# Kernel optimization log

Measured on AMD Instinct MI355X. Metric: run time of the kernel, lower is better.

## Reference

```python
import jax, jax.numpy as jnp
import numpy as np

WS = 7          # window_size
DIM = 384
H = 12          # num_heads
N = WS * WS     # tokens per window
NW = 64         # number of windows (attn_mask.shape[0])
B_ = 4096       # window-batch; divisible by NW


def _relative_position_index(ws: int) -> np.ndarray:
    coords = np.stack(np.meshgrid(np.arange(ws), np.arange(ws), indexing='ij'))  # (2, ws, ws)
    flat = coords.reshape(2, -1)                                                 # (2, N)
    rel = flat[:, :, None] - flat[:, None, :]                                    # (2, N, N)
    rel = rel.transpose(1, 2, 0).astype(np.int64)                                # (N, N, 2)
    rel[:, :, 0] += ws - 1
    rel[:, :, 1] += ws - 1
    rel[:, :, 0] *= 2 * ws - 1
    return rel.sum(-1)                                                           # (N, N)

REL_IDX = jnp.asarray(_relative_position_index(WS))


def setup_inputs() -> dict:
    key = jax.random.key(0)
    ks = jax.random.split(key, 7)
    return {
        'x': jax.random.normal(ks[0], (B_, N, DIM), jnp.float32),
        'attn_mask': jax.random.normal(ks[1], (NW, N, N), jnp.float32),
        'qkv_w': jax.random.normal(ks[2], (3 * DIM, DIM), jnp.float32) * 0.02,
        'qkv_b': jax.random.normal(ks[3], (3 * DIM,), jnp.float32) * 0.02,
        'proj_w': jax.random.normal(ks[4], (DIM, DIM), jnp.float32) * 0.02,
        'proj_b': jax.random.normal(ks[5], (DIM,), jnp.float32) * 0.02,
        'rpb_table': jax.random.normal(ks[6], ((2 * WS - 1) ** 2, H), jnp.float32) * 0.02,
    }


def reference(x, attn_mask, qkv_w, qkv_b, proj_w, proj_b, rpb_table):
    b, n, c = x.shape
    hd = c // H
    scale = hd ** (-0.5)
    qkv = x @ qkv_w.T + qkv_b                                  # (B_, N, 3C)
    qkv = qkv.reshape(b, n, 3, H, hd).transpose(2, 0, 3, 1, 4)  # (3, B_, H, N, hd)
    q, k, v = qkv[0] * scale, qkv[1], qkv[2]
    attn = jnp.einsum('bhnd,bhmd->bhnm', q, k)                 # (B_, H, N, N)
    bias = rpb_table[REL_IDX]                                  # (N, N, H)
    attn = attn + bias.transpose(2, 0, 1)[None]
    nw = attn_mask.shape[0]
    attn = attn.reshape(b // nw, nw, H, n, n) + attn_mask[None, :, None]
    attn = jax.nn.softmax(attn.reshape(b, H, n, n), axis=-1)
    out = jnp.einsum('bhnm,bhmd->bhnd', attn, v)               # (B_, H, N, hd)
    out = out.transpose(0, 2, 1, 3).reshape(b, n, c)
    return out @ proj_w.T + proj_b
```

## Files before the change

### kernel.cpp

```cpp
#include <hip/hip_runtime.h>

#define TOKS 49
#define DIM_ 384
#define NHEAD 12

typedef short bf16x8 __attribute__((ext_vector_type(8)));
typedef float f32x4 __attribute__((ext_vector_type(4)));

#define SXA 392
#define SQK 136
#define SV   72

#define LDS_ELEMS (64*SXA + 64*SQK + 64*SQK + 128*SV + 64*SXA)
#define LDS_BYTES (LDS_ELEMS*2)

#define W1E (3*DIM_*DIM_)
#define W2E (DIM_*DIM_)
#define CMBE (64*NHEAD*64*64)
#define WS_NEEDED ((size_t)(W1E+W2E)*2 + (size_t)CMBE*4)

__device__ __forceinline__ unsigned short f2b(float f) {
  union { float f; unsigned u; } x; x.f = f;
  return (unsigned short)((x.u + 0x7FFFu + ((x.u >> 16) & 1u)) >> 16);
}

__device__ __forceinline__ unsigned pack2(float lo, float hi) {
  return (unsigned)f2b(lo) | ((unsigned)f2b(hi) << 16);
}

__global__ void prep_kernel(const float* __restrict__ qkv_w,
                            const float* __restrict__ proj_w,
                            const float* __restrict__ rpb,
                            const float* __restrict__ mask,
                            unsigned short* __restrict__ w1p,
                            unsigned short* __restrict__ w2p,
                            float* __restrict__ cmb) {
  int i = blockIdx.x * 256 + threadIdx.x;
  if (i < W1E) {
    int j = i & 7, l = (i >> 3) & 63, rest = i >> 9;
    int kk = rest % 12, ct = rest / 12;
    w1p[i] = f2b(qkv_w[(ct*16 + (l & 15))*DIM_ + kk*32 + ((l >> 4) << 3) + j]);
  }
  if (i < W2E) {
    int j = i & 7, l = (i >> 3) & 63, rest = i >> 9;
    int kk = rest % 12, ct = rest / 12;
    w2p[i] = f2b(proj_w[(ct*16 + (l & 15))*DIM_ + kk*32 + ((l >> 4) << 3) + j]);
  }
  if (i < CMBE) {
    int k = i & 63, q = (i >> 6) & 63, hw = i >> 12;
    int h = hw % 12, wi = hw / 12;
    float v = -1e30f;
    if (q < TOKS && k < TOKS) {
      int idx = (q/7 - k/7 + 6)*13 + (q%7 - k%7 + 6);
      v = rpb[idx*NHEAD + h] + mask[((size_t)wi*TOKS + q)*TOKS + k];
    }
    cmb[i] = v;
  }
}

__global__ __launch_bounds__(1024, 1)
void wattn_kernel(const float* __restrict__ x,
                  const unsigned short* __restrict__ w1p,
                  const float* __restrict__ b1,
                  const unsigned short* __restrict__ w2p,
                  const float* __restrict__ b2,
                  const float* __restrict__ cmb,
                  float* __restrict__ out) {
  extern __shared__ unsigned short lds[];
  unsigned short* xA  = lds;
  unsigned short* Q4  = xA + 64*SXA;
  unsigned short* K4  = Q4 + 64*SQK;
  unsigned short* Vt4 = K4 + 64*SQK;
  unsigned short* Ob  = Vt4 + 128*SV;

  const int tid  = threadIdx.x;
  const int lane = tid & 63;
  const int wv   = tid >> 6;
  const int lr   = lane & 15;
  const int lg   = lane >> 4;
  const int b    = blockIdx.x;
  const int wi   = b & 63;

  const int mh    = wv & 1;
  const int ctile = wv >> 1;

  {
    const float* xg = x + (size_t)b * TOKS * DIM_;
    for (int idx = tid; idx < TOKS*48; idx += 1024) {
      int r = idx / 48, c8 = (idx % 48) << 3;
      const float4* p = (const float4*)(xg + r*DIM_ + c8);
      float4 a0 = p[0], a1 = p[1];
      uint4 w;
      w.x = pack2(a0.x, a0.y); w.y = pack2(a0.z, a0.w);
      w.z = pack2(a1.x, a1.y); w.w = pack2(a1.z, a1.w);
      *(uint4*)&xA[r*SXA + c8] = w;
    }
    uint4 z = {0,0,0,0};
    for (int idx = tid; idx < 15*48; idx += 1024) {
      int r = 49 + idx / 48, c8 = (idx % 48) << 3;
      *(uint4*)&xA[r*SXA + c8] = z;
    }
  }
  __syncthreads();

  const f32x4 fz = {0.f, 0.f, 0.f, 0.f};
  f32x4 aq[2], ak[2], av[2];

  auto g1c = [&](int gg) {
    const int cb = gg*8 + ctile;
    const unsigned short* bq = w1p + (size_t)(cb*12)*512 + (lane << 3);
    const unsigned short* bk = bq + (size_t)(24*12)*512;
    const unsigned short* bv = bq + (size_t)(48*12)*512;
    #pragma unroll
    for (int t = 0; t < 2; ++t) { aq[t] = fz; ak[t] = fz; av[t] = fz; }
    #pragma unroll
    for (int kk = 0; kk < 12; ++kk) {
      bf16x8 fq = *(const bf16x8*)(bq + kk*512);
      bf16x8 fk = *(const bf16x8*)(bk + kk*512);
      bf16x8 fv = *(const bf16x8*)(bv + kk*512);
      #pragma unroll
      for (int t = 0; t < 2; ++t) {
        bf16x8 a = *(const bf16x8*)&xA[((mh*2 + t)*16 + lr)*SXA + kk*32 + lg*8];
        aq[t] = __builtin_amdgcn_mfma_f32_16x16x32_bf16(fq, a, aq[t], 0, 0, 0);
        ak[t] = __builtin_amdgcn_mfma_f32_16x16x32_bf16(fk, a, ak[t], 0, 0, 0);
        av[t] = __builtin_amdgcn_mfma_f32_16x16x32_bf16(a, fv, av[t], 0, 0, 0);
      }
    }
  };

  auto g1w = [&](int gg) {
    const int cb = gg*8 + ctile;
    const f32x4 qb4 = *(const f32x4*)(b1 + cb*16 + (lg << 2));
    const f32x4 kb4 = *(const f32x4*)(b1 + (24 + cb)*16 + (lg << 2));
    const float bsv = b1[(48 + cb)*16 + lr];
    const int d128 = (ctile << 4) + lr;
    #pragma unroll
    for (int t = 0; t < 2; ++t) {
      const int tokr = mh*32 + t*16 + lr;
      uint2 qw, kw, vw;
      qw.x = pack2((aq[t][0] + qb4[0]) * 0.17677669529663687f,
                   (aq[t][1] + qb4[1]) * 0.17677669529663687f);
      qw.y = pack2((aq[t][2] + qb4[2]) * 0.17677669529663687f,
                   (aq[t][3] + qb4[3]) * 0.17677669529663687f);
      kw.x = pack2(ak[t][0] + kb4[0], ak[t][1] + kb4[1]);
      kw.y = pack2(ak[t][2] + kb4[2], ak[t][3] + kb4[3]);
      vw.x = pack2(av[t][0] + bsv, av[t][1] + bsv);
      vw.y = pack2(av[t][2] + bsv, av[t][3] + bsv);
      *(uint2*)&Q4[tokr*SQK + (ctile << 4) + (lg << 2)] = qw;
      *(uint2*)&K4[tokr*SQK + (ctile << 4) + (lg << 2)] = kw;
      *(uint2*)&Vt4[d128*SV + mh*32 + t*16 + (lg << 2)] = vw;
    }
  };

  for (int g = 0; g < 3; ++g) {
    g1c(g);
    g1w(g);
    __syncthreads();

    const int hl = wv >> 2;
    const int h  = g*4 + hl;
    const int qoff = hl * 32;
    const int m0 = (wv & 3) << 4;

    f32x4 c4[4];
    const float* cp = cmb + (((size_t)(wi*NHEAD + h)) << 12) + ((m0 + lr) << 6);
    #pragma unroll
    for (int nt = 0; nt < 4; ++nt)
      c4[nt] = *(const f32x4*)(cp + nt*16 + (lg << 2));

    bf16x8 qa = *(const bf16x8*)&Q4[(m0 + lr)*SQK + qoff + lg*8];
    f32x4 S[4];
    #pragma unroll
    for (int nt = 0; nt < 4; ++nt) {
      bf16x8 kb = *(const bf16x8*)&K4[((nt << 4) + lr)*SQK + qoff + lg*8];
      S[nt] = __builtin_amdgcn_mfma_f32_16x16x32_bf16(kb, qa, fz, 0, 0, 0);
    }

    float p[4][4];
    float mx = -1e30f;
    #pragma unroll
    for (int nt = 0; nt < 4; ++nt)
      #pragma unroll
      for (int jj = 0; jj < 4; ++jj) {
        p[nt][jj] = S[nt][jj] + c4[nt][jj];
        mx = fmaxf(mx, p[nt][jj]);
      }
    mx = fmaxf(mx, __shfl_xor(mx, 16));
    mx = fmaxf(mx, __shfl_xor(mx, 32));
    float sum = 0.f;
    #pragma unroll
    for (int nt = 0; nt < 4; ++nt)
      #pragma unroll
      for (int jj = 0; jj < 4; ++jj) {
        float e = __expf(p[nt][jj] - mx);
        p[nt][jj] = e; sum += e;
      }
    sum += __shfl_xor(sum, 16);
    sum += __shfl_xor(sum, 32);
    const float inv = 1.0f / sum;

    unsigned pk0[4], pk1[4];
    #pragma unroll
    for (int nt = 0; nt < 4; ++nt) {
      pk0[nt] = pack2(p[nt][0]*inv, p[nt][1]*inv);
      pk1[nt] = pack2(p[nt][2]*inv, p[nt][3]*inv);
    }

    const int src0 = lr + ((lane & 16) << 1);
    const int src1 = src0 + 16;
    const bool loH = lane < 32;
    f32x4 o0 = fz, o1 = fz;
    #pragma unroll
    for (int kk = 0; kk < 2; ++kk) {
      unsigned wA0 = __shfl(pk0[2*kk], src0), wB0 = __shfl(pk0[2*kk+1], src0);
      unsigned wA1 = __shfl(pk1[2*kk], src0), wB1 = __shfl(pk1[2*kk+1], src0);
      unsigned wA2 = __shfl(pk0[2*kk], src1), wB2 = __shfl(pk0[2*kk+1], src1);
      unsigned wA3 = __shfl(pk1[2*kk], src1), wB3 = __shfl(pk1[2*kk+1], src1);
      union { unsigned u[4]; bf16x8 v; } af;
      af.u[0] = loH ? wA0 : wB0;
      af.u[1] = loH ? wA1 : wB1;
      af.u[2] = loH ? wA2 : wB2;
      af.u[3] = loH ? wA3 : wB3;
      bf16x8 vb0 = *(const bf16x8*)&Vt4[(qoff + lr)*SV + kk*32 + lg*8];
      bf16x8 vb1 = *(const bf16x8*)&Vt4[(qoff + 16 + lr)*SV + kk*32 + lg*8];
      o0 = __builtin_amdgcn_mfma_f32_16x16x32_bf16(vb0, af.v, o0, 0, 0, 0);
      o1 = __builtin_amdgcn_mfma_f32_16x16x32_bf16(vb1, af.v, o1, 0, 0, 0);
    }
    const int orow = m0 + lr;
    uint2 w0, w1;
    w0.x = pack2(o0[0], o0[1]); w0.y = pack2(o0[2], o0[3]);
    w1.x = pack2(o1[0], o1[1]); w1.y = pack2(o1[2], o1[3]);
    *(uint2*)&Ob[orow*SXA + h*32 + (lg << 2)]      = w0;
    *(uint2*)&Ob[orow*SXA + h*32 + 16 + (lg << 2)] = w1;

    __syncthreads();
  }

  {
    const unsigned short* bp0 = w2p + (size_t)(ctile*12)*512 + (lane << 3);
    const unsigned short* bp1 = bp0 + (size_t)(8*12)*512;
    const unsigned short* bp2 = bp0 + (size_t)(16*12)*512;
    f32x4 ac0[2], ac1[2], ac2[2];
    #pragma unroll
    for (int t = 0; t < 2; ++t) { ac0[t] = fz; ac1[t] = fz; ac2[t] = fz; }
    #pragma unroll
    for (int kk = 0; kk < 12; ++kk) {
      bf16x8 f0 = *(const bf16x8*)(bp0 + kk*512);
      bf16x8 f1 = *(const bf16x8*)(bp1 + kk*512);
      bf16x8 f2 = *(const bf16x8*)(bp2 + kk*512);
      #pragma unroll
      for (int t = 0; t < 2; ++t) {
        bf16x8 ob = *(const bf16x8*)&Ob[((mh*2 + t)*16 + lr)*SXA + kk*32 + lg*8];
        ac0[t] = __builtin_amdgcn_mfma_f32_16x16x32_bf16(f0, ob, ac0[t], 0, 0, 0);
        ac1[t] = __builtin_amdgcn_mfma_f32_16x16x32_bf16(f1, ob, ac1[t], 0, 0, 0);
        ac2[t] = __builtin_amdgcn_mfma_f32_16x16x32_bf16(f2, ob, ac2[t], 0, 0, 0);
      }
    }
    float* og = out + (size_t)b * TOKS * DIM_;
    #pragma unroll
    for (int ni = 0; ni < 3; ++ni) {
      const int col0 = ((ctile + ni*8) << 4) + (lg << 2);
      const f32x4 pb = *(const f32x4*)(b2 + col0);
      const f32x4* ac = ni == 0 ? ac0 : (ni == 1 ? ac1 : ac2);
      #pragma unroll
      for (int t = 0; t < 2; ++t) {
        const int tok = (mh*2 + t)*16 + lr;
        if (tok < TOKS) {
          f32x4 v = ac[t] + pb;
          *(f32x4*)(og + tok*DIM_ + col0) = v;
        }
      }
    }
  }
}

extern "C" void kernel_launch(void* const* d_in, const int* in_sizes, int n_in,
                              void* d_out, int out_size, void* d_ws, size_t ws_size,
                              hipStream_t stream) {
  const float* x      = (const float*)d_in[0];
  const float* mask   = (const float*)d_in[1];
  const float* qkv_w  = (const float*)d_in[2];
  const float* qkv_b  = (const float*)d_in[3];
  const float* proj_w = (const float*)d_in[4];
  const float* proj_b = (const float*)d_in[5];
  const float* rpb    = (const float*)d_in[6];
  float* out = (float*)d_out;

  if (ws_size < WS_NEEDED) return;

  unsigned short* w1p = (unsigned short*)d_ws;
  unsigned short* w2p = w1p + W1E;
  float* cmb = (float*)(w2p + W2E);

  prep_kernel<<<(CMBE + 255)/256, 256, 0, stream>>>(qkv_w, proj_w, rpb, mask,
                                                    w1p, w2p, cmb);

  hipFuncSetAttribute((const void*)wattn_kernel,
                      hipFuncAttributeMaxDynamicSharedMemorySize, LDS_BYTES);
  wattn_kernel<<<4096, 1024, LDS_BYTES, stream>>>(x, w1p, qkv_b, w2p,
                                                  proj_b, cmb, out);
}
```

Measured before the change: 606.0 us.

## Shrink blocks to 512 threads and interleave per-head projection accumulation

Blocks drop from 1024 to 512 threads and process two heads per step across six steps instead of four heads across three. The output projection is no longer a final pass over a full attention-output buffer. It is accumulated step by step from a small per-step buffer that reuses the Q region, which shrinks LDS so several blocks can share a CU. The cost is more barriers per step, more accumulator registers per thread, and repeated small weight loads for the projection.

```diff
diff --git a/kernel.cpp b/kernel.cpp
--- a/kernel.cpp
+++ b/kernel.cpp
@@ -8,10 +8,9 @@
 typedef float f32x4 __attribute__((ext_vector_type(4)));
 
 #define SXA 392
-#define SQK 136
-#define SV   72
-
-#define LDS_ELEMS (64*SXA + 64*SQK + 64*SQK + 128*SV + 64*SXA)
+#define SQ  72
+
+#define LDS_ELEMS (64*SXA + 3*64*SQ)
 #define LDS_BYTES (LDS_ELEMS*2)
 
 #define W1E (3*DIM_*DIM_)
@@ -23,7 +22,6 @@
   union { float f; unsigned u; } x; x.f = f;
   return (unsigned short)((x.u + 0x7FFFu + ((x.u >> 16) & 1u)) >> 16);
 }
-
 __device__ __forceinline__ unsigned pack2(float lo, float hi) {
   return (unsigned)f2b(lo) | ((unsigned)f2b(hi) << 16);
 }
@@ -58,7 +56,7 @@
   }
 }
 
-__global__ __launch_bounds__(1024, 1)
+__global__ __launch_bounds__(512, 4)
 void wattn_kernel(const float* __restrict__ x,
                   const unsigned short* __restrict__ w1p,
                   const float* __restrict__ b1,
@@ -68,10 +66,10 @@
                   float* __restrict__ out) {
   extern __shared__ unsigned short lds[];
   unsigned short* xA  = lds;
-  unsigned short* Q4  = xA + 64*SXA;
-  unsigned short* K4  = Q4 + 64*SQK;
-  unsigned short* Vt4 = K4 + 64*SQK;
-  unsigned short* Ob  = Vt4 + 128*SV;
+  unsigned short* Q2  = xA + 64*SXA;
+  unsigned short* K2  = Q2 + 64*SQ;
+  unsigned short* Vt2 = K2 + 64*SQ;
+  unsigned short* ObG = Q2;
 
   const int tid  = threadIdx.x;
   const int lane = tid & 63;
@@ -81,12 +79,14 @@
   const int b    = blockIdx.x;
   const int wi   = b & 63;
 
-  const int mh    = wv & 1;
-  const int ctile = wv >> 1;
+  const int ct2 = wv >> 1;
+  const int mh  = wv & 1;
+  const int hl  = wv >> 2;
+  const int m0  = (wv & 3) << 4;
 
   {
     const float* xg = x + (size_t)b * TOKS * DIM_;
-    for (int idx = tid; idx < TOKS*48; idx += 1024) {
+    for (int idx = tid; idx < TOKS*48; idx += 512) {
       int r = idx / 48, c8 = (idx % 48) << 3;
       const float4* p = (const float4*)(xg + r*DIM_ + c8);
       float4 a0 = p[0], a1 = p[1];
@@ -96,7 +96,7 @@
       *(uint4*)&xA[r*SXA + c8] = w;
     }
     uint4 z = {0,0,0,0};
-    for (int idx = tid; idx < 15*48; idx += 1024) {
+    for (int idx = tid; idx < 15*48; idx += 512) {
       int r = 49 + idx / 48, c8 = (idx % 48) << 3;
       *(uint4*)&xA[r*SXA + c8] = z;
     }
@@ -104,63 +104,57 @@
   __syncthreads();
 
   const f32x4 fz = {0.f, 0.f, 0.f, 0.f};
-  f32x4 aq[2], ak[2], av[2];
-
-  auto g1c = [&](int gg) {
-    const int cb = gg*8 + ctile;
-    const unsigned short* bq = w1p + (size_t)(cb*12)*512 + (lane << 3);
-    const unsigned short* bk = bq + (size_t)(24*12)*512;
-    const unsigned short* bv = bq + (size_t)(48*12)*512;
-    #pragma unroll
-    for (int t = 0; t < 2; ++t) { aq[t] = fz; ak[t] = fz; av[t] = fz; }
-    #pragma unroll
-    for (int kk = 0; kk < 12; ++kk) {
-      bf16x8 fq = *(const bf16x8*)(bq + kk*512);
-      bf16x8 fk = *(const bf16x8*)(bk + kk*512);
-      bf16x8 fv = *(const bf16x8*)(bv + kk*512);
+  f32x4 ac0[4], ac1[4], ac2[4];
+  #pragma unroll
+  for (int m = 0; m < 4; ++m) { ac0[m]=fz; ac1[m]=fz; ac2[m]=fz; }
+
+  for (int g = 0; g < 6; ++g) {
+    {
+      const int cb = g*4 + ct2;
+      const unsigned short* bq = w1p + (size_t)(cb*12)*512 + (lane << 3);
+      const unsigned short* bk = bq + (size_t)(24*12)*512;
+      const unsigned short* bv = bq + (size_t)(48*12)*512;
+      f32x4 aq[2], ak[2], av[2];
+      #pragma unroll
+      for (int t = 0; t < 2; ++t) { aq[t]=fz; ak[t]=fz; av[t]=fz; }
+      #pragma unroll
+      for (int kk = 0; kk < 12; ++kk) {
+        bf16x8 fq = *(const bf16x8*)(bq + kk*512);
+        bf16x8 fk = *(const bf16x8*)(bk + kk*512);
+        bf16x8 fv = *(const bf16x8*)(bv + kk*512);
+        #pragma unroll
+        for (int t = 0; t < 2; ++t) {
+          bf16x8 a = *(const bf16x8*)&xA[((mh*2 + t)*16 + lr)*SXA + kk*32 + lg*8];
+          aq[t] = __builtin_amdgcn_mfma_f32_16x16x32_bf16(fq, a, aq[t], 0, 0, 0);
+          ak[t] = __builtin_amdgcn_mfma_f32_16x16x32_bf16(fk, a, ak[t], 0, 0, 0);
+          av[t] = __builtin_amdgcn_mfma_f32_16x16x32_bf16(a, fv, av[t], 0, 0, 0);
+        }
+      }
+      const f32x4 qb4 = *(const f32x4*)(b1 + cb*16 + (lg << 2));
+      const f32x4 kb4 = *(const f32x4*)(b1 + (24 + cb)*16 + (lg << 2));
+      const float bsv = b1[(48 + cb)*16 + lr];
+      const int d64 = (ct2 << 4) + lr;
       #pragma unroll
       for (int t = 0; t < 2; ++t) {
-        bf16x8 a = *(const bf16x8*)&xA[((mh*2 + t)*16 + lr)*SXA + kk*32 + lg*8];
-        aq[t] = __builtin_amdgcn_mfma_f32_16x16x32_bf16(fq, a, aq[t], 0, 0, 0);
-        ak[t] = __builtin_amdgcn_mfma_f32_16x16x32_bf16(fk, a, ak[t], 0, 0, 0);
-        av[t] = __builtin_amdgcn_mfma_f32_16x16x32_bf16(a, fv, av[t], 0, 0, 0);
-      }
-    }
-  };
-
-  auto g1w = [&](int gg) {
-    const int cb = gg*8 + ctile;
-    const f32x4 qb4 = *(const f32x4*)(b1 + cb*16 + (lg << 2));
-    const f32x4 kb4 = *(const f32x4*)(b1 + (24 + cb)*16 + (lg << 2));
-    const float bsv = b1[(48 + cb)*16 + lr];
-    const int d128 = (ctile << 4) + lr;
-    #pragma unroll
-    for (int t = 0; t < 2; ++t) {
-      const int tokr = mh*32 + t*16 + lr;
-      uint2 qw, kw, vw;
-      qw.x = pack2((aq[t][0] + qb4[0]) * 0.17677669529663687f,
-                   (aq[t][1] + qb4[1]) * 0.17677669529663687f);
-      qw.y = pack2((aq[t][2] + qb4[2]) * 0.17677669529663687f,
-                   (aq[t][3] + qb4[3]) * 0.17677669529663687f);
-      kw.x = pack2(ak[t][0] + kb4[0], ak[t][1] + kb4[1]);
-      kw.y = pack2(ak[t][2] + kb4[2], ak[t][3] + kb4[3]);
-      vw.x = pack2(av[t][0] + bsv, av[t][1] + bsv);
-      vw.y = pack2(av[t][2] + bsv, av[t][3] + bsv);
-      *(uint2*)&Q4[tokr*SQK + (ctile << 4) + (lg << 2)] = qw;
-      *(uint2*)&K4[tokr*SQK + (ctile << 4) + (lg << 2)] = kw;
-      *(uint2*)&Vt4[d128*SV + mh*32 + t*16 + (lg << 2)] = vw;
-    }
-  };
-
-  for (int g = 0; g < 3; ++g) {
-    g1c(g);
-    g1w(g);
-    __syncthreads();
-
-    const int hl = wv >> 2;
-    const int h  = g*4 + hl;
+        const int tokr = mh*32 + t*16 + lr;
+        uint2 qw, kw, vw;
+        qw.x = pack2((aq[t][0] + qb4[0]) * 0.17677669529663687f,
+                     (aq[t][1] + qb4[1]) * 0.17677669529663687f);
+        qw.y = pack2((aq[t][2] + qb4[2]) * 0.17677669529663687f,
+                     (aq[t][3] + qb4[3]) * 0.17677669529663687f);
+        kw.x = pack2(ak[t][0] + kb4[0], ak[t][1] + kb4[1]);
+        kw.y = pack2(ak[t][2] + kb4[2], ak[t][3] + kb4[3]);
+        vw.x = pack2(av[t][0] + bsv, av[t][1] + bsv);
+        vw.y = pack2(av[t][2] + bsv, av[t][3] + bsv);
+        *(uint2*)&Q2[tokr*SQ + (ct2 << 4) + (lg << 2)] = qw;
+        *(uint2*)&K2[tokr*SQ + (ct2 << 4) + (lg << 2)] = kw;
+        *(uint2*)&Vt2[d64*SQ + mh*32 + t*16 + (lg << 2)] = vw;
+      }
+    }
+    __syncthreads();
+
+    const int h = g*2 + hl;
     const int qoff = hl * 32;
-    const int m0 = (wv & 3) << 4;
 
     f32x4 c4[4];
     const float* cp = cmb + (((size_t)(wi*NHEAD + h)) << 12) + ((m0 + lr) << 6);
@@ -168,11 +162,11 @@
     for (int nt = 0; nt < 4; ++nt)
       c4[nt] = *(const f32x4*)(cp + nt*16 + (lg << 2));
 
-    bf16x8 qa = *(const bf16x8*)&Q4[(m0 + lr)*SQK + qoff + lg*8];
+    bf16x8 qa = *(const bf16x8*)&Q2[(m0 + lr)*SQ + qoff + lg*8];
     f32x4 S[4];
     #pragma unroll
     for (int nt = 0; nt < 4; ++nt) {
-      bf16x8 kb = *(const bf16x8*)&K4[((nt << 4) + lr)*SQK + qoff + lg*8];
+      bf16x8 kb = *(const bf16x8*)&K2[((nt << 4) + lr)*SQ + qoff + lg*8];
       S[nt] = __builtin_amdgcn_mfma_f32_16x16x32_bf16(kb, qa, fz, 0, 0, 0);
     }
 
@@ -205,68 +199,71 @@
       pk0[nt] = pack2(p[nt][0]*inv, p[nt][1]*inv);
       pk1[nt] = pack2(p[nt][2]*inv, p[nt][3]*inv);
     }
-
-    const int src0 = lr + ((lane & 16) << 1);
-    const int src1 = src0 + 16;
-    const bool loH = lane < 32;
-    f32x4 o0 = fz, o1 = fz;
-    #pragma unroll
-    for (int kk = 0; kk < 2; ++kk) {
-      unsigned wA0 = __shfl(pk0[2*kk], src0), wB0 = __shfl(pk0[2*kk+1], src0);
-      unsigned wA1 = __shfl(pk1[2*kk], src0), wB1 = __shfl(pk1[2*kk+1], src0);
-      unsigned wA2 = __shfl(pk0[2*kk], src1), wB2 = __shfl(pk0[2*kk+1], src1);
-      unsigned wA3 = __shfl(pk1[2*kk], src1), wB3 = __shfl(pk1[2*kk+1], src1);
-      union { unsigned u[4]; bf16x8 v; } af;
-      af.u[0] = loH ? wA0 : wB0;
-      af.u[1] = loH ? wA1 : wB1;
-      af.u[2] = loH ? wA2 : wB2;
-      af.u[3] = loH ? wA3 : wB3;
-      bf16x8 vb0 = *(const bf16x8*)&Vt4[(qoff + lr)*SV + kk*32 + lg*8];
-      bf16x8 vb1 = *(const bf16x8*)&Vt4[(qoff + 16 + lr)*SV + kk*32 + lg*8];
-      o0 = __builtin_amdgcn_mfma_f32_16x16x32_bf16(vb0, af.v, o0, 0, 0, 0);
-      o1 = __builtin_amdgcn_mfma_f32_16x16x32_bf16(vb1, af.v, o1, 0, 0, 0);
-    }
-    const int orow = m0 + lr;
-    uint2 w0, w1;
-    w0.x = pack2(o0[0], o0[1]); w0.y = pack2(o0[2], o0[3]);
-    w1.x = pack2(o1[0], o1[1]); w1.y = pack2(o1[2], o1[3]);
-    *(uint2*)&Ob[orow*SXA + h*32 + (lg << 2)]      = w0;
-    *(uint2*)&Ob[orow*SXA + h*32 + 16 + (lg << 2)] = w1;
-
+    __syncthreads();
+
+    {
+      const int src0 = lr + ((lane & 16) << 1);
+      const int src1 = src0 + 16;
+      const bool loH = lane < 32;
+      f32x4 o0 = fz, o1 = fz;
+      #pragma unroll
+      for (int kk = 0; kk < 2; ++kk) {
+        unsigned wA0 = __shfl(pk0[2*kk], src0), wB0 = __shfl(pk0[2*kk+1], src0);
+        unsigned wA1 = __shfl(pk1[2*kk], src0), wB1 = __shfl(pk1[2*kk+1], src0);
+        unsigned wA2 = __shfl(pk0[2*kk], src1), wB2 = __shfl(pk0[2*kk+1], src1);
+        unsigned wA3 = __shfl(pk1[2*kk], src1), wB3 = __shfl(pk1[2*kk+1], src1);
+        union { unsigned u[4]; bf16x8 v; } af;
+        af.u[0] = loH ? wA0 : wB0;
+        af.u[1] = loH ? wA1 : wB1;
+        af.u[2] = loH ? wA2 : wB2;
+        af.u[3] = loH ? wA3 : wB3;
+        bf16x8 vb0 = *(const bf16x8*)&Vt2[(qoff + lr)*SQ + kk*32 + lg*8];
+        bf16x8 vb1 = *(const bf16x8*)&Vt2[(qoff + 16 + lr)*SQ + kk*32 + lg*8];
+        o0 = __builtin_amdgcn_mfma_f32_16x16x32_bf16(vb0, af.v, o0, 0, 0, 0);
+        o1 = __builtin_amdgcn_mfma_f32_16x16x32_bf16(vb1, af.v, o1, 0, 0, 0);
+      }
+      const int orow = m0 + lr;
+      uint2 w0, w1;
+      w0.x = pack2(o0[0], o0[1]); w0.y = pack2(o0[2], o0[3]);
+      w1.x = pack2(o1[0], o1[1]); w1.y = pack2(o1[2], o1[3]);
+      *(uint2*)&ObG[orow*SQ + hl*32 + (lg << 2)]      = w0;
+      *(uint2*)&ObG[orow*SQ + hl*32 + 16 + (lg << 2)] = w1;
+    }
+    __syncthreads();
+
+    {
+      #pragma unroll
+      for (int kkg = 0; kkg < 2; ++kkg) {
+        const unsigned short* f0p = w2p + (size_t)((wv)*12 + 2*g + kkg)*512 + (lane << 3);
+        const unsigned short* f1p = w2p + (size_t)((wv+8)*12 + 2*g + kkg)*512 + (lane << 3);
+        const unsigned short* f2p = w2p + (size_t)((wv+16)*12 + 2*g + kkg)*512 + (lane << 3);
+        bf16x8 f0 = *(const bf16x8*)f0p;
+        bf16x8 f1 = *(const bf16x8*)f1p;
+        bf16x8 f2 = *(const bf16x8*)f2p;
+        #pragma unroll
+        for (int m = 0; m < 4; ++m) {
+          bf16x8 ob = *(const bf16x8*)&ObG[(m*16 + lr)*SQ + kkg*32 + lg*8];
+          ac0[m] = __builtin_amdgcn_mfma_f32_16x16x32_bf16(f0, ob, ac0[m], 0, 0, 0);
+          ac1[m] = __builtin_amdgcn_mfma_f32_16x16x32_bf16(f1, ob, ac1[m], 0, 0, 0);
+          ac2[m] = __builtin_amdgcn_mfma_f32_16x16x32_bf16(f2, ob, ac2[m], 0, 0, 0);
+        }
+      }
+    }
     __syncthreads();
   }
 
   {
-    const unsigned short* bp0 = w2p + (size_t)(ctile*12)*512 + (lane << 3);
-    const unsigned short* bp1 = bp0 + (size_t)(8*12)*512;
-    const unsigned short* bp2 = bp0 + (size_t)(16*12)*512;
-    f32x4 ac0[2], ac1[2], ac2[2];
-    #pragma unroll
-    for (int t = 0; t < 2; ++t) { ac0[t] = fz; ac1[t] = fz; ac2[t] = fz; }
-    #pragma unroll
-    for (int kk = 0; kk < 12; ++kk) {
-      bf16x8 f0 = *(const bf16x8*)(bp0 + kk*512);
-      bf16x8 f1 = *(const bf16x8*)(bp1 + kk*512);
-      bf16x8 f2 = *(const bf16x8*)(bp2 + kk*512);
-      #pragma unroll
-      for (int t = 0; t < 2; ++t) {
-        bf16x8 ob = *(const bf16x8*)&Ob[((mh*2 + t)*16 + lr)*SXA + kk*32 + lg*8];
-        ac0[t] = __builtin_amdgcn_mfma_f32_16x16x32_bf16(f0, ob, ac0[t], 0, 0, 0);
-        ac1[t] = __builtin_amdgcn_mfma_f32_16x16x32_bf16(f1, ob, ac1[t], 0, 0, 0);
-        ac2[t] = __builtin_amdgcn_mfma_f32_16x16x32_bf16(f2, ob, ac2[t], 0, 0, 0);
-      }
-    }
     float* og = out + (size_t)b * TOKS * DIM_;
     #pragma unroll
     for (int ni = 0; ni < 3; ++ni) {
-      const int col0 = ((ctile + ni*8) << 4) + (lg << 2);
+      const int col0 = ((wv + ni*8) << 4) + (lg << 2);
       const f32x4 pb = *(const f32x4*)(b2 + col0);
       const f32x4* ac = ni == 0 ? ac0 : (ni == 1 ? ac1 : ac2);
       #pragma unroll
-      for (int t = 0; t < 2; ++t) {
-        const int tok = (mh*2 + t)*16 + lr;
+      for (int m = 0; m < 4; ++m) {
+        const int tok = m*16 + lr;
         if (tok < TOKS) {
-          f32x4 v = ac[t] + pb;
+          f32x4 v = ac[m] + pb;
           *(f32x4*)(og + tok*DIM_ + col0) = v;
         }
       }
@@ -297,6 +294,6 @@
 
   hipFuncSetAttribute((const void*)wattn_kernel,
                       hipFuncAttributeMaxDynamicSharedMemorySize, LDS_BYTES);
-  wattn_kernel<<<4096, 1024, LDS_BYTES, stream>>>(x, w1p, qkv_b, w2p,
-                                                  proj_b, cmb, out);
-}
+  wattn_kernel<<<4096, 512, LDS_BYTES, stream>>>(x, w1p, qkv_b, w2p,
+                                                 proj_b, cmb, out);
+}
```

After: 827.8 us. +36.6%, slower.
